# Kernel optimization log

Hardware: AMD Instinct MI355X
Metric: run time of the kernel (lower is better)

## Reference

```python
import jax, jax.numpy as jnp
import numpy as np

H = W = 256
C = 128
SCALE = 512 ** (-0.5)  # literal from the source, not 1/sqrt(C)


def _pool_mat(size, out):
    # adaptive_avg_pool1d matrix: row i averages input[start_i:end_i]
    i = np.arange(out)
    s = (i * size) // out
    e = ((i + 1) * size + out - 1) // out  # ceil
    P = np.zeros((out, size), np.float32)
    for k in range(out):
        P[k, s[k]:e[k]] = 1.0 / (e[k] - s[k])
    return jnp.asarray(P)


def adaptive_avg_pool2d(x, out):
    # x: [B, C, H, W] -> [B, C, out, out] via separable pooling matrices
    Ph = _pool_mat(x.shape[2], out)
    Pw = _pool_mat(x.shape[3], out)
    y = jnp.einsum('oh,bchw->bcow', Ph, x)
    return jnp.einsum('pw,bcow->bcop', Pw, y)


def setup_inputs() -> dict:
    key = jax.random.key(0)
    k1, k2 = jax.random.split(key)
    x5 = jax.random.normal(k1, (4, C, H, W), dtype=jnp.float32)
    W_out = jax.random.normal(k2, (C, C), dtype=jnp.float32) * 0.02
    b_out = jnp.zeros((C,), dtype=jnp.float32)
    return {"x5": x5, "W_out": W_out, "b_out": b_out}


def reference(x5, W_out, b_out):
    B = x5.shape[0]
    # Query: [B, N, C], N = H*W
    Query = x5.reshape(B, C, H * W).transpose(0, 2, 1)
    # multi-scale pooled keys
    p16 = adaptive_avg_pool2d(x5, 16)
    p12 = adaptive_avg_pool2d(x5, 12)
    p9 = adaptive_avg_pool2d(x5, 9)
    p7 = adaptive_avg_pool2d(x5, 7)
    p6 = adaptive_avg_pool2d(x5, 6)
    p3 = adaptive_avg_pool2d(x5, 3)
    p1 = adaptive_avg_pool2d(x5, 1)
    # Key: concat flattened pools in source order [3, 1, 9, 7, 16] -> [B, C, 396]
    Key = jnp.concatenate(
        [p.reshape(B, C, -1) for p in (p3, p1, p9, p7, p16)], axis=-1)
    Value = Key.transpose(0, 2, 1)  # [B, 396, C]
    # attention: [B, N, 396]
    attn = jax.nn.softmax(SCALE * jnp.einsum('bnc,bck->bnk', Query, Key), axis=-1)
    agg = jnp.einsum('bnk,bkc->bnc', attn, Value)  # [B, N, C]
    agg = agg.transpose(0, 2, 1).reshape(B, C, H, W)
    # 1x1 conv
    out = jnp.einsum('oc,bchw->bohw', W_out, agg) + b_out[None, :, None, None]
    return (out + x5, p12, p6)
```

## Files before the change

### kernel.cpp

```cpp
#include <hip/hip_runtime.h>
#include <hip/hip_bf16.h>

typedef short bf16x8 __attribute__((ext_vector_type(8)));
typedef float f32x4  __attribute__((ext_vector_type(4)));
typedef unsigned short u16;

#define B_N 4
#define C_N 128
#define HW_ 256
#define NPIX 65536
#define NK 396
#define NKP 400
#define OUT_MAIN ((size_t)B_N * C_N * NPIX)
#define P12_OFF OUT_MAIN
#define P6_OFF  (P12_OFF + (size_t)B_N * C_N * 144)

#define BUFSZ  32768
#define VT_OFF 16384
#define P_OFF  65536
#define LDS_BYTES 73728

static __device__ __forceinline__ u16 f2bf(float x) {
  __hip_bfloat16 h = __float2bfloat16(x);
  return *(u16*)&h;
}
static __device__ __forceinline__ unsigned pack2(float lo, float hi) {
  return ((unsigned)f2bf(hi) << 16) | f2bf(lo);
}
static __device__ __forceinline__ void gl_lds16(const void* g, void* l) {
  __builtin_amdgcn_global_load_lds(
      (const __attribute__((address_space(1))) unsigned*)g,
      (__attribute__((address_space(3))) unsigned*)l, 16, 0, 0);
}
#define MFMA32 __builtin_amdgcn_mfma_f32_16x16x32_bf16
#define LGKM0 do { asm volatile("s_waitcnt lgkmcnt(0)" ::: "memory"); \
                   __builtin_amdgcn_sched_barrier(0); } while (0)

__global__ __launch_bounds__(1024) void pool_kernel(
    const float* __restrict__ x5, const float* __restrict__ W_out,
    u16* __restrict__ wsK, u16* __restrict__ wsKT, u16* __restrict__ wsW,
    float* __restrict__ out)
{
  __shared__ float yh[54][257];
  const int tid = threadIdx.x;
  const int bc = blockIdx.x;
  const int b  = bc >> 7;
  const int c  = bc & 127;
  const float2* plane2 = (const float2*)(x5 + (size_t)bc * NPIX);
  const int w2 = tid & 127;
  const int q  = tid >> 7;
  const int h0 = q * 32;

  if (bc < 16) {
    const int idx = bc * 1024 + tid;
    wsW[idx] = f2bf(W_out[idx]);
  }

  for (int i = tid; i < 54 * 257; i += 1024) ((float*)yh)[i] = 0.f;
  __syncthreads();

  const int os_[7] = {16,12,9,7,6,3,1};
  const int ro_[7] = {0,16,28,37,44,50,53};
  float ax[7], ay[7], a2x[7], a2y[7], inv_[7];
  int r_[7], e_[7], s2_[7];
  #pragma unroll
  for (int s = 0; s < 7; ++s) {
    const int o = os_[s];
    const int r = (h0 * o) >> 8;
    const int sr = (r * 256) / o;
    r_[s]  = r;
    e_[s]  = ((r + 1) * 256 + o - 1) / o;
    s2_[s] = ((r + 1) * 256) / o;
    inv_[s] = 1.0f / (float)(e_[s] - sr);
    ax[s] = 0.f; ay[s] = 0.f; a2x[s] = 0.f; a2y[s] = 0.f;
  }

  for (int h = h0; h < h0 + 32; ++h) {
    const float2 v = plane2[h * 128 + w2];
    #pragma unroll
    for (int s = 0; s < 7; ++s) {
      const int o = os_[s];
      ax[s] += v.x; ay[s] += v.y;
      if (h >= s2_[s]) { a2x[s] += v.x; a2y[s] += v.y; }
      if (h + 1 == e_[s]) {
        atomicAdd(&yh[ro_[s] + r_[s]][2*w2],     ax[s] * inv_[s]);
        atomicAdd(&yh[ro_[s] + r_[s]][2*w2 + 1], ay[s] * inv_[s]);
        r_[s]++;
        const int sr = s2_[s];
        e_[s]  = ((r_[s] + 1) * 256 + o - 1) / o;
        s2_[s] = ((r_[s] + 1) * 256) / o;
        inv_[s] = 1.0f / (float)(e_[s] - sr);
        ax[s] = a2x[s]; ay[s] = a2y[s];
        a2x[s] = 0.f; a2y[s] = 0.f;
      }
    }
  }
  #pragma unroll
  for (int s = 0; s < 7; ++s) {
    const int o = os_[s];
    if (r_[s] < o) {
      atomicAdd(&yh[ro_[s] + r_[s]][2*w2],     ax[s] * inv_[s]);
      atomicAdd(&yh[ro_[s] + r_[s]][2*w2 + 1], ay[s] * inv_[s]);
      if (r_[s] + 1 < o && s2_[s] < h0 + 32) {
        const int sr2 = s2_[s];
        const int e2  = ((r_[s] + 2) * 256 + o - 1) / o;
        const float inv2 = 1.0f / (float)(e2 - sr2);
        atomicAdd(&yh[ro_[s] + r_[s] + 1][2*w2],     a2x[s] * inv2);
        atomicAdd(&yh[ro_[s] + r_[s] + 1][2*w2 + 1], a2y[s] * inv2);
      }
    }
  }
  __syncthreads();

  if (tid < NKP - NK) {
    wsK [((size_t)b * NKP + NK + tid) * C_N + c] = 0;
    wsKT[(size_t)bc * NKP + NK + tid] = 0;
  }

  for (int r = tid; r < 576; r += 1024) {
    int rr = r;
    int o, ro, kbase, dst;
    if      (rr < 256) { o = 16; ro = 0;  kbase = 140; dst = 0; }
    else if (rr < 400) { o = 12; ro = 16; kbase = 0;   dst = 1; rr -= 256; }
    else if (rr < 481) { o = 9;  ro = 28; kbase = 10;  dst = 0; rr -= 400; }
    else if (rr < 530) { o = 7;  ro = 37; kbase = 91;  dst = 0; rr -= 481; }
    else if (rr < 566) { o = 6;  ro = 44; kbase = 0;   dst = 2; rr -= 530; }
    else if (rr < 575) { o = 3;  ro = 50; kbase = 0;   dst = 0; rr -= 566; }
    else               { o = 1;  ro = 53; kbase = 9;   dst = 0; rr = 0;   }
    const int i = rr / o;
    const int j = rr - i * o;
    const int s = (j * HW_) / o;
    const int e = ((j + 1) * HW_ + o - 1) / o;
    float sum = 0.f;
    const float* row = yh[ro + i];
    for (int wq = s; wq < e; ++wq) sum += row[wq];
    const float v = sum * (1.0f / (float)(e - s));
    if (dst == 1) {
      out[P12_OFF + (size_t)bc * 144 + rr] = v;
    } else if (dst == 2) {
      out[P6_OFF + (size_t)bc * 36 + rr] = v;
    } else {
      const int key = kbase + rr;
      const u16 bv = f2bf(v);
      wsK [((size_t)b * NKP + key) * C_N + c] = bv;
      wsKT[(size_t)bc * NKP + key]            = bv;
    }
  }
}

template<int CB, int BUF>
static __device__ __forceinline__ void stage64(
    char* smem, const char* wsKb, const char* wsKTb, int wv, int lane)
{
  char* buf = smem + BUF * BUFSZ;
  #pragma unroll
  for (int j = 0; j < 4; ++j) {
    const int krow = CB + j*16 + wv*4 + (lane >> 4);
    gl_lds16(wsKb + (size_t)krow * 256 + (((lane & 15) ^ (krow & 15)) << 4),
             buf + j*4096 + wv*1024);
    const int vrow = j*32 + wv*8 + (lane >> 3);
    gl_lds16(wsKTb + (size_t)vrow * (NKP*2) + CB*2 + (((lane & 7) ^ (vrow & 7)) << 4),
             buf + VT_OFF + j*4096 + wv*1024);
  }
}

static __device__ __forceinline__ void stage_tail(
    char* buf, const char* wsKb, const char* wsKTb, int wv, int lane)
{
  {
    const int row = wv*4 + (lane >> 4);
    gl_lds16(wsKb + (size_t)(384 + row) * 256 + (((lane & 15) ^ (row & 15)) << 4),
             buf + wv * 1024);
  }
  #pragma unroll
  for (int j = 0; j < 2; ++j) {
    const int row = j*64 + wv*16 + (lane >> 2);
    gl_lds16(wsKTb + (size_t)row * (NKP*2) + 768 + ((lane & 3) << 4),
             buf + VT_OFF + j*4096 + wv*1024);
  }
}

static __device__ __forceinline__ void stage_W(
    char* smem, const u16* wsW, int wv, int lane)
{
  #pragma unroll
  for (int j = 0; j < 8; ++j) {
    const int row = j*16 + wv*4 + (lane >> 4);
    gl_lds16((const char*)wsW + (size_t)row * 256 + (((lane & 15) ^ (row & 15)) << 4),
             smem + BUFSZ + j*4096 + wv*1024);
  }
}

template<int BUF, int TAIL>
static __device__ __forceinline__ void compute64(
    char* smem, char* pbase, const bf16x8 (&qf)[2][4],
    f32x4 (&agg)[8][2], float (&d)[2], int l15, int l4)
{
  const char* buf = smem + BUF * BUFSZ;
  constexpr int NT   = TAIL ? 1 : 4;
  constexpr int SUBS = TAIL ? 1 : 2;
  const float SCL2 = 0.044194173824159216f * 1.4426950408889634f;

  f32x4 sA[NT][2];
  #pragma unroll
  for (int nt = 0; nt < NT; ++nt) {
    sA[nt][0] = (f32x4){0.f,0.f,0.f,0.f};
    sA[nt][1] = (f32x4){0.f,0.f,0.f,0.f};
  }
  #pragma unroll
  for (int nt = 0; nt < NT; ++nt) {
    bf16x8 kf[4];
    #pragma unroll
    for (int kc = 0; kc < 4; ++kc)
      kf[kc] = *(const bf16x8*)(buf + (nt*16 + l15) * 256 +
                                ((kc*64 + l4*16) ^ (l15 << 4)));
    #pragma unroll
    for (int kc = 0; kc < 4; ++kc) {
      sA[nt][0] = MFMA32(kf[kc], qf[0][kc], sA[nt][0], 0, 0, 0);
      sA[nt][1] = MFMA32(kf[kc], qf[1][kc], sA[nt][1], 0, 0, 0);
    }
  }

  #pragma unroll
  for (int sub = 0; sub < SUBS; ++sub) {
    if (sub) LGKM0;
    #pragma unroll
    for (int pt = 0; pt < 2; ++pt) {
      const int prow = pt*16 + l15;
      const int sz2  = (prow & 3) << 4;
      #pragma unroll
      for (int u = 0; u < (TAIL ? 1 : 2); ++u) {
        const int nt = sub*2 + u;
        float p[4];
        #pragma unroll
        for (int qi = 0; qi < 4; ++qi) {
          float e = exp2f(sA[nt][pt][qi] * SCL2);
          if (TAIL && (l4*4 + qi >= 12)) e = 0.f;
          p[qi] = e;
        }
        d[pt] += (p[0] + p[1]) + (p[2] + p[3]);
        uint2 pk;
        pk.x = pack2(p[0], p[1]);
        pk.y = pack2(p[2], p[3]);
        *(uint2*)(pbase + prow*64 + ((u*32 + l4*8) ^ sz2)) = pk;
      }
      if (TAIL) {
        uint2 z; z.x = 0u; z.y = 0u;
        *(uint2*)(pbase + prow*64 + ((32 + l4*8) ^ sz2)) = z;
      }
    }
    LGKM0;

    bf16x8 pf[2];
    #pragma unroll
    for (int pt = 0; pt < 2; ++pt) {
      const int prow = pt*16 + l15;
      pf[pt] = *(const bf16x8*)(pbase + prow*64 + ((l4*16) ^ ((prow & 3) << 4)));
    }
    #pragma unroll
    for (int ct = 0; ct < 8; ++ct) {
      const int vrow = ct*16 + l15;
      bf16x8 vf;
      if (TAIL)
        vf = *(const bf16x8*)(buf + VT_OFF + vrow*64 + l4*16);
      else
        vf = *(const bf16x8*)(buf + VT_OFF + vrow*128 +
                              ((sub*64 + l4*16) ^ ((vrow & 7) << 4)));
      agg[ct][0] = MFMA32(vf, pf[0], agg[ct][0], 0, 0, 0);
      agg[ct][1] = MFMA32(vf, pf[1], agg[ct][1], 0, 0, 0);
    }
  }
}

__global__ __launch_bounds__(256, 2) void attn_kernel(
    const float* __restrict__ x5, const u16* __restrict__ wsK,
    const u16* __restrict__ wsKT, const u16* __restrict__ wsW,
    const float* __restrict__ b_out, float* __restrict__ out)
{
  extern __shared__ char smem[];
  const int tid  = threadIdx.x;
  const int b    = blockIdx.x >> 9;
  const int pix0 = (blockIdx.x & 511) << 7;
  const int lane = tid & 63, wv = tid >> 6;
  const int l15  = lane & 15, l4 = lane >> 4;
  char* pbase = smem + P_OFF + wv * 2048;

  const char* wsKb  = (const char*)wsK  + (size_t)b * NKP * C_N * 2;
  const char* wsKTb = (const char*)wsKT + (size_t)b * C_N * NKP * 2;

  {
    const float* r0p = x5 + (((size_t)(b * C_N + 2*lane)) << 16) + pix0 + wv * 32;
    const float* r1p = r0p + NPIX;
    float4 v0[8], v1[8];
    #pragma unroll
    for (int j = 0; j < 8; ++j) {
      v0[j] = *(const float4*)(r0p + j*4);
      v1[j] = *(const float4*)(r1p + j*4);
    }
    #pragma unroll
    for (int i = 0; i < 32; ++i) {
      const int pix = wv * 32 + i;
      const unsigned pk = pack2(((const float*)&v0[i>>2])[i&3],
                                ((const float*)&v1[i>>2])[i&3]);
      *(unsigned*)(smem + pix * 256 + ((lane*4) ^ ((pix & 15) << 4))) = pk;
    }
  }
  __syncthreads();

  bf16x8 qf[2][4];
  #pragma unroll
  for (int pt = 0; pt < 2; ++pt)
    #pragma unroll
    for (int kc = 0; kc < 4; ++kc)
      qf[pt][kc] = *(const bf16x8*)(smem + (wv*32 + pt*16 + l15) * 256 +
                                    ((kc*64 + l4*16) ^ (l15 << 4)));
  __syncthreads();

  f32x4 agg[8][2];
  #pragma unroll
  for (int ct = 0; ct < 8; ++ct) {
    agg[ct][0] = (f32x4){0.f,0.f,0.f,0.f};
    agg[ct][1] = (f32x4){0.f,0.f,0.f,0.f};
  }
  float d[2] = {0.f, 0.f};

  stage64<0, 0>(smem, wsKb, wsKTb, wv, lane);
  asm volatile("s_waitcnt vmcnt(0)" ::: "memory");
  __syncthreads();

  stage64<64, 1>(smem, wsKb, wsKTb, wv, lane);
  compute64<0, 0>(smem, pbase, qf, agg, d, l15, l4);
  asm volatile("s_waitcnt vmcnt(0)" ::: "memory");
  __syncthreads();

  stage64<128, 0>(smem, wsKb, wsKTb, wv, lane);
  compute64<1, 0>(smem, pbase, qf, agg, d, l15, l4);
  asm volatile("s_waitcnt vmcnt(0)" ::: "memory");
  __syncthreads();

  stage64<192, 1>(smem, wsKb, wsKTb, wv, lane);
  compute64<0, 0>(smem, pbase, qf, agg, d, l15, l4);
  asm volatile("s_waitcnt vmcnt(0)" ::: "memory");
  __syncthreads();

  stage64<256, 0>(smem, wsKb, wsKTb, wv, lane);
  compute64<1, 0>(smem, pbase, qf, agg, d, l15, l4);
  asm volatile("s_waitcnt vmcnt(0)" ::: "memory");
  __syncthreads();

  stage64<320, 1>(smem, wsKb, wsKTb, wv, lane);
  compute64<0, 0>(smem, pbase, qf, agg, d, l15, l4);
  asm volatile("s_waitcnt vmcnt(0)" ::: "memory");
  __syncthreads();

  stage_tail(smem, wsKb, wsKTb, wv, lane);
  compute64<1, 0>(smem, pbase, qf, agg, d, l15, l4);
  asm volatile("s_waitcnt vmcnt(0)" ::: "memory");
  __syncthreads();

  {
    f32x4 z = (f32x4){0.f,0.f,0.f,0.f};
    *(f32x4*)(smem + VT_OFF + (tid >> 1) * 64 + 32 + ((tid & 1) << 4)) = z;
  }
  stage_W(smem, wsW, wv, lane);
  asm volatile("s_waitcnt vmcnt(0)" ::: "memory");
  __syncthreads();

  compute64<0, 1>(smem, pbase, qf, agg, d, l15, l4);

  float inv[2];
  #pragma unroll
  for (int pt = 0; pt < 2; ++pt) {
    float s = d[pt];
    s += __shfl_xor(s, 16);
    s += __shfl_xor(s, 32);
    inv[pt] = 1.0f / s;
  }

  f32x4 cacc[8][2];
  #pragma unroll
  for (int ot = 0; ot < 8; ++ot) {
    cacc[ot][0] = (f32x4){0.f,0.f,0.f,0.f};
    cacc[ot][1] = (f32x4){0.f,0.f,0.f,0.f};
  }
  #pragma unroll
  for (int qh = 0; qh < 4; ++qh) {
    LGKM0;
    #pragma unroll
    for (int pt = 0; pt < 2; ++pt) {
      const int prow = pt*16 + l15;
      const int sz2  = (prow & 3) << 4;
      #pragma unroll
      for (int u = 0; u < 2; ++u) {
        const f32x4 a = agg[qh*2 + u][pt];
        uint2 pk;
        pk.x = pack2(a[0] * inv[pt], a[1] * inv[pt]);
        pk.y = pack2(a[2] * inv[pt], a[3] * inv[pt]);
        *(uint2*)(pbase + prow*64 + ((u*32 + l4*8) ^ sz2)) = pk;
      }
    }
    LGKM0;
    bf16x8 agf[2];
    #pragma unroll
    for (int pt = 0; pt < 2; ++pt) {
      const int prow = pt*16 + l15;
      agf[pt] = *(const bf16x8*)(pbase + prow*64 + ((l4*16) ^ ((prow & 3) << 4)));
    }
    #pragma unroll
    for (int ot = 0; ot < 8; ++ot) {
      const bf16x8 wa = *(const bf16x8*)(smem + BUFSZ + (ot*16 + l15) * 256 +
                                         ((qh*64 + l4*16) ^ (l15 << 4)));
      cacc[ot][0] = MFMA32(wa, agf[0], cacc[ot][0], 0, 0, 0);
      cacc[ot][1] = MFMA32(wa, agf[1], cacc[ot][1], 0, 0, 0);
    }
  }

  #pragma unroll
  for (int ot = 0; ot < 8; ++ot) {
    const float4 bq = *(const float4*)(b_out + ot*16 + l4*4);
    #pragma unroll
    for (int pt = 0; pt < 2; ++pt) {
      #pragma unroll
      for (int qi = 0; qi < 4; ++qi) {
        const int o = ot*16 + l4*4 + qi;
        const size_t idx = (((size_t)(b * C_N + o)) << 16) + pix0 + wv*32 + pt*16 + l15;
        out[idx] = cacc[ot][pt][qi] + ((const float*)&bq)[qi] + x5[idx];
      }
    }
  }
}

extern "C" void kernel_launch(void* const* d_in, const int* in_sizes, int n_in,
                              void* d_out, int out_size, void* d_ws, size_t ws_size,
                              hipStream_t stream) {
  const float* x5    = (const float*)d_in[0];
  const float* W_out = (const float*)d_in[1];
  const float* b_out = (const float*)d_in[2];
  float* out = (float*)d_out;
  u16* wsKT = (u16*)d_ws;
  u16* wsK  = (u16*)((char*)d_ws + (size_t)B_N * C_N * NKP * 2);
  u16* wsW  = (u16*)((char*)d_ws + (size_t)2 * B_N * C_N * NKP * 2);

  pool_kernel<<<512, 1024, 0, stream>>>(x5, W_out, wsK, wsKT, wsW, out);

  hipFuncSetAttribute((const void*)attn_kernel,
                      hipFuncAttributeMaxDynamicSharedMemorySize, LDS_BYTES);
  attn_kernel<<<B_N * 512, 256, LDS_BYTES, stream>>>(x5, wsK, wsKT, wsW, b_out, out);
}
```

Baseline: 213.1 us.

## Halve key chunk size to cut LDS use and raise attention occupancy

The attention kernel now streams keys and values in 32-key chunks instead of 64-key chunks, which halves the LDS buffers (about 40 KB total) and raises launch bounds from 2 to 4 blocks per CU. The W_out matrix is no longer staged in LDS. It is stored in a K-blocked bf16 layout and read straight from global memory during the 1x1 conv epilogue. The pooling kernel also batches eight row loads before accumulating, to expose more memory parallelism. The trade-off is twice as many barrier/stage steps and uncached global reads of W that rely on the L2 cache.

```diff
diff --git a/kernel.cpp b/kernel.cpp
--- a/kernel.cpp
+++ b/kernel.cpp
@@ -15,10 +15,10 @@
 #define P12_OFF OUT_MAIN
 #define P6_OFF  (P12_OFF + (size_t)B_N * C_N * 144)
 
-#define BUFSZ  32768
-#define VT_OFF 16384
-#define P_OFF  65536
-#define LDS_BYTES 73728
+#define BUFSZ  16384
+#define VT_OFF 8192
+#define P_OFF  32768
+#define LDS_BYTES 40960
 
 static __device__ __forceinline__ u16 f2bf(float x) {
   __hip_bfloat16 h = __float2bfloat16(x);
@@ -53,7 +53,8 @@
 
   if (bc < 16) {
     const int idx = bc * 1024 + tid;
-    wsW[idx] = f2bf(W_out[idx]);
+    const int o = idx >> 7, cc = idx & 127;
+    wsW[(cc >> 5) * 4096 + o * 32 + (cc & 31)] = f2bf(W_out[idx]);
   }
 
   for (int i = tid; i < 54 * 257; i += 1024) ((float*)yh)[i] = 0.f;
@@ -75,23 +76,31 @@
     ax[s] = 0.f; ay[s] = 0.f; a2x[s] = 0.f; a2y[s] = 0.f;
   }
 
-  for (int h = h0; h < h0 + 32; ++h) {
-    const float2 v = plane2[h * 128 + w2];
-    #pragma unroll
-    for (int s = 0; s < 7; ++s) {
-      const int o = os_[s];
-      ax[s] += v.x; ay[s] += v.y;
-      if (h >= s2_[s]) { a2x[s] += v.x; a2y[s] += v.y; }
-      if (h + 1 == e_[s]) {
-        atomicAdd(&yh[ro_[s] + r_[s]][2*w2],     ax[s] * inv_[s]);
-        atomicAdd(&yh[ro_[s] + r_[s]][2*w2 + 1], ay[s] * inv_[s]);
-        r_[s]++;
-        const int sr = s2_[s];
-        e_[s]  = ((r_[s] + 1) * 256 + o - 1) / o;
-        s2_[s] = ((r_[s] + 1) * 256) / o;
-        inv_[s] = 1.0f / (float)(e_[s] - sr);
-        ax[s] = a2x[s]; ay[s] = a2y[s];
-        a2x[s] = 0.f; a2y[s] = 0.f;
+  #pragma unroll
+  for (int g = 0; g < 4; ++g) {
+    float2 vv[8];
+    #pragma unroll
+    for (int k = 0; k < 8; ++k) vv[k] = plane2[(h0 + g*8 + k) * 128 + w2];
+    #pragma unroll
+    for (int k = 0; k < 8; ++k) {
+      const int h = h0 + g*8 + k;
+      const float2 v = vv[k];
+      #pragma unroll
+      for (int s = 0; s < 7; ++s) {
+        const int o = os_[s];
+        ax[s] += v.x; ay[s] += v.y;
+        if (h >= s2_[s]) { a2x[s] += v.x; a2y[s] += v.y; }
+        if (h + 1 == e_[s]) {
+          atomicAdd(&yh[ro_[s] + r_[s]][2*w2],     ax[s] * inv_[s]);
+          atomicAdd(&yh[ro_[s] + r_[s]][2*w2 + 1], ay[s] * inv_[s]);
+          r_[s]++;
+          const int sr = s2_[s];
+          e_[s]  = ((r_[s] + 1) * 256 + o - 1) / o;
+          s2_[s] = ((r_[s] + 1) * 256) / o;
+          inv_[s] = 1.0f / (float)(e_[s] - sr);
+          ax[s] = a2x[s]; ay[s] = a2y[s];
+          a2x[s] = 0.f; a2y[s] = 0.f;
+        }
       }
     }
   }
@@ -149,17 +158,17 @@
 }
 
 template<int CB, int BUF>
-static __device__ __forceinline__ void stage64(
+static __device__ __forceinline__ void stage32(
     char* smem, const char* wsKb, const char* wsKTb, int wv, int lane)
 {
   char* buf = smem + BUF * BUFSZ;
   #pragma unroll
-  for (int j = 0; j < 4; ++j) {
-    const int krow = CB + j*16 + wv*4 + (lane >> 4);
-    gl_lds16(wsKb + (size_t)krow * 256 + (((lane & 15) ^ (krow & 15)) << 4),
+  for (int j = 0; j < 2; ++j) {
+    const int kr = j*16 + wv*4 + (lane >> 4);
+    gl_lds16(wsKb + (size_t)(CB + kr) * 256 + (((lane & 15) ^ (kr & 15)) << 4),
              buf + j*4096 + wv*1024);
-    const int vrow = j*32 + wv*8 + (lane >> 3);
-    gl_lds16(wsKTb + (size_t)vrow * (NKP*2) + CB*2 + (((lane & 7) ^ (vrow & 7)) << 4),
+    const int vr = j*64 + wv*16 + (lane >> 2);
+    gl_lds16(wsKTb + (size_t)vr * (NKP*2) + CB*2 + (((lane & 3) ^ (vr & 3)) << 4),
              buf + VT_OFF + j*4096 + wv*1024);
   }
 }
@@ -180,25 +189,13 @@
   }
 }
 
-static __device__ __forceinline__ void stage_W(
-    char* smem, const u16* wsW, int wv, int lane)
-{
-  #pragma unroll
-  for (int j = 0; j < 8; ++j) {
-    const int row = j*16 + wv*4 + (lane >> 4);
-    gl_lds16((const char*)wsW + (size_t)row * 256 + (((lane & 15) ^ (row & 15)) << 4),
-             smem + BUFSZ + j*4096 + wv*1024);
-  }
-}
-
 template<int BUF, int TAIL>
-static __device__ __forceinline__ void compute64(
+static __device__ __forceinline__ void compute32(
     char* smem, char* pbase, const bf16x8 (&qf)[2][4],
     f32x4 (&agg)[8][2], float (&d)[2], int l15, int l4)
 {
   const char* buf = smem + BUF * BUFSZ;
-  constexpr int NT   = TAIL ? 1 : 4;
-  constexpr int SUBS = TAIL ? 1 : 2;
+  constexpr int NT = TAIL ? 1 : 2;
   const float SCL2 = 0.044194173824159216f * 1.4426950408889634f;
 
   f32x4 sA[NT][2];
@@ -222,57 +219,59 @@
   }
 
   #pragma unroll
-  for (int sub = 0; sub < SUBS; ++sub) {
-    if (sub) LGKM0;
-    #pragma unroll
-    for (int pt = 0; pt < 2; ++pt) {
-      const int prow = pt*16 + l15;
-      const int sz2  = (prow & 3) << 4;
+  for (int pt = 0; pt < 2; ++pt) {
+    const int prow = pt*16 + l15;
+    const int sz2  = (prow & 3) << 4;
+    #pragma unroll
+    for (int nt = 0; nt < NT; ++nt) {
+      float p[4];
       #pragma unroll
-      for (int u = 0; u < (TAIL ? 1 : 2); ++u) {
-        const int nt = sub*2 + u;
-        float p[4];
-        #pragma unroll
-        for (int qi = 0; qi < 4; ++qi) {
-          float e = exp2f(sA[nt][pt][qi] * SCL2);
-          if (TAIL && (l4*4 + qi >= 12)) e = 0.f;
-          p[qi] = e;
-        }
-        d[pt] += (p[0] + p[1]) + (p[2] + p[3]);
-        uint2 pk;
-        pk.x = pack2(p[0], p[1]);
-        pk.y = pack2(p[2], p[3]);
-        *(uint2*)(pbase + prow*64 + ((u*32 + l4*8) ^ sz2)) = pk;
+      for (int qi = 0; qi < 4; ++qi) {
+        float e = exp2f(sA[nt][pt][qi] * SCL2);
+        if (TAIL && (l4*4 + qi >= 12)) e = 0.f;
+        p[qi] = e;
       }
-      if (TAIL) {
-        uint2 z; z.x = 0u; z.y = 0u;
-        *(uint2*)(pbase + prow*64 + ((32 + l4*8) ^ sz2)) = z;
-      }
-    }
-    LGKM0;
-
-    bf16x8 pf[2];
-    #pragma unroll
-    for (int pt = 0; pt < 2; ++pt) {
-      const int prow = pt*16 + l15;
-      pf[pt] = *(const bf16x8*)(pbase + prow*64 + ((l4*16) ^ ((prow & 3) << 4)));
-    }
-    #pragma unroll
-    for (int ct = 0; ct < 8; ++ct) {
-      const int vrow = ct*16 + l15;
-      bf16x8 vf;
-      if (TAIL)
-        vf = *(const bf16x8*)(buf + VT_OFF + vrow*64 + l4*16);
-      else
-        vf = *(const bf16x8*)(buf + VT_OFF + vrow*128 +
-                              ((sub*64 + l4*16) ^ ((vrow & 7) << 4)));
-      agg[ct][0] = MFMA32(vf, pf[0], agg[ct][0], 0, 0, 0);
-      agg[ct][1] = MFMA32(vf, pf[1], agg[ct][1], 0, 0, 0);
-    }
-  }
-}
-
-__global__ __launch_bounds__(256, 2) void attn_kernel(
+      d[pt] += (p[0] + p[1]) + (p[2] + p[3]);
+      uint2 pk;
+      pk.x = pack2(p[0], p[1]);
+      pk.y = pack2(p[2], p[3]);
+      *(uint2*)(pbase + prow*64 + ((nt*32 + l4*8) ^ sz2)) = pk;
+    }
+    if (TAIL) {
+      uint2 z; z.x = 0u; z.y = 0u;
+      *(uint2*)(pbase + prow*64 + ((32 + l4*8) ^ sz2)) = z;
+    }
+  }
+  LGKM0;
+
+  bf16x8 pf[2];
+  #pragma unroll
+  for (int pt = 0; pt < 2; ++pt) {
+    const int prow = pt*16 + l15;
+    pf[pt] = *(const bf16x8*)(pbase + prow*64 + ((l4*16) ^ ((prow & 3) << 4)));
+  }
+  #pragma unroll
+  for (int ct = 0; ct < 8; ++ct) {
+    const int vrow = ct*16 + l15;
+    bf16x8 vf;
+    if (TAIL)
+      vf = *(const bf16x8*)(buf + VT_OFF + vrow*64 + l4*16);
+    else
+      vf = *(const bf16x8*)(buf + VT_OFF + vrow*64 + ((l4*16) ^ ((vrow & 3) << 4)));
+    agg[ct][0] = MFMA32(vf, pf[0], agg[ct][0], 0, 0, 0);
+    agg[ct][1] = MFMA32(vf, pf[1], agg[ct][1], 0, 0, 0);
+  }
+}
+
+#define CHUNK_STEP(I, STAGENEXT)                                   \
+  do {                                                             \
+    STAGENEXT;                                                     \
+    compute32<(I) & 1, 0>(smem, pbase, qf, agg, d, l15, l4);       \
+    asm volatile("s_waitcnt vmcnt(0)" ::: "memory");               \
+    __syncthreads();                                               \
+  } while (0)
+
+__global__ __launch_bounds__(256, 4) void attn_kernel(
     const float* __restrict__ x5, const u16* __restrict__ wsK,
     const u16* __restrict__ wsKT, const u16* __restrict__ wsW,
     const float* __restrict__ b_out, float* __restrict__ out)
@@ -324,49 +323,30 @@
   }
   float d[2] = {0.f, 0.f};
 
-  stage64<0, 0>(smem, wsKb, wsKTb, wv, lane);
+  stage32<0, 0>(smem, wsKb, wsKTb, wv, lane);
   asm volatile("s_waitcnt vmcnt(0)" ::: "memory");
   __syncthreads();
 
-  stage64<64, 1>(smem, wsKb, wsKTb, wv, lane);
-  compute64<0, 0>(smem, pbase, qf, agg, d, l15, l4);
-  asm volatile("s_waitcnt vmcnt(0)" ::: "memory");
-  __syncthreads();
-
-  stage64<128, 0>(smem, wsKb, wsKTb, wv, lane);
-  compute64<1, 0>(smem, pbase, qf, agg, d, l15, l4);
-  asm volatile("s_waitcnt vmcnt(0)" ::: "memory");
-  __syncthreads();
-
-  stage64<192, 1>(smem, wsKb, wsKTb, wv, lane);
-  compute64<0, 0>(smem, pbase, qf, agg, d, l15, l4);
-  asm volatile("s_waitcnt vmcnt(0)" ::: "memory");
-  __syncthreads();
-
-  stage64<256, 0>(smem, wsKb, wsKTb, wv, lane);
-  compute64<1, 0>(smem, pbase, qf, agg, d, l15, l4);
-  asm volatile("s_waitcnt vmcnt(0)" ::: "memory");
-  __syncthreads();
-
-  stage64<320, 1>(smem, wsKb, wsKTb, wv, lane);
-  compute64<0, 0>(smem, pbase, qf, agg, d, l15, l4);
-  asm volatile("s_waitcnt vmcnt(0)" ::: "memory");
-  __syncthreads();
-
-  stage_tail(smem, wsKb, wsKTb, wv, lane);
-  compute64<1, 0>(smem, pbase, qf, agg, d, l15, l4);
-  asm volatile("s_waitcnt vmcnt(0)" ::: "memory");
-  __syncthreads();
+  CHUNK_STEP(0,  (stage32<32,  1>(smem, wsKb, wsKTb, wv, lane)));
+  CHUNK_STEP(1,  (stage32<64,  0>(smem, wsKb, wsKTb, wv, lane)));
+  CHUNK_STEP(2,  (stage32<96,  1>(smem, wsKb, wsKTb, wv, lane)));
+  CHUNK_STEP(3,  (stage32<128, 0>(smem, wsKb, wsKTb, wv, lane)));
+  CHUNK_STEP(4,  (stage32<160, 1>(smem, wsKb, wsKTb, wv, lane)));
+  CHUNK_STEP(5,  (stage32<192, 0>(smem, wsKb, wsKTb, wv, lane)));
+  CHUNK_STEP(6,  (stage32<224, 1>(smem, wsKb, wsKTb, wv, lane)));
+  CHUNK_STEP(7,  (stage32<256, 0>(smem, wsKb, wsKTb, wv, lane)));
+  CHUNK_STEP(8,  (stage32<288, 1>(smem, wsKb, wsKTb, wv, lane)));
+  CHUNK_STEP(9,  (stage32<320, 0>(smem, wsKb, wsKTb, wv, lane)));
+  CHUNK_STEP(10, (stage32<352, 1>(smem, wsKb, wsKTb, wv, lane)));
+  CHUNK_STEP(11, (stage_tail(smem, wsKb, wsKTb, wv, lane)));
 
   {
     f32x4 z = (f32x4){0.f,0.f,0.f,0.f};
     *(f32x4*)(smem + VT_OFF + (tid >> 1) * 64 + 32 + ((tid & 1) << 4)) = z;
   }
-  stage_W(smem, wsW, wv, lane);
-  asm volatile("s_waitcnt vmcnt(0)" ::: "memory");
-  __syncthreads();
-
-  compute64<0, 1>(smem, pbase, qf, agg, d, l15, l4);
+  __syncthreads();
+
+  compute32<0, 1>(smem, pbase, qf, agg, d, l15, l4);
 
   float inv[2];
   #pragma unroll
@@ -406,10 +386,10 @@
       const int prow = pt*16 + l15;
       agf[pt] = *(const bf16x8*)(pbase + prow*64 + ((l4*16) ^ ((prow & 3) << 4)));
     }
+    const u16* Wq = wsW + qh * 4096;
     #pragma unroll
     for (int ot = 0; ot < 8; ++ot) {
-      const bf16x8 wa = *(const bf16x8*)(smem + BUFSZ + (ot*16 + l15) * 256 +
-                                         ((qh*64 + l4*16) ^ (l15 << 4)));
+      const bf16x8 wa = *(const bf16x8*)(Wq + (ot*16 + l15) * 32 + l4*8);
       cacc[ot][0] = MFMA32(wa, agf[0], cacc[ot][0], 0, 0, 0);
       cacc[ot][1] = MFMA32(wa, agf[1], cacc[ot][1], 0, 0, 0);
     }
```

Result: slower. 497.7 us (+133.5%).
